# Kernel tuning notes

Hardware: AMD Instinct MI355X
Metric: run time of the kernel (lower is better)

Reference implementation:

```python
import jax, jax.numpy as jnp
import numpy as np
from jax import lax

DN = ('NCHW', 'OIHW', 'NCHW')

def conv2d(x, w, b=None, padding='SAME'):
    y = lax.conv_general_dilated(x, w, (1, 1), padding, dimension_numbers=DN)
    if b is not None:
        y = y + b[None, :, None, None]
    return y

def setup_inputs() -> dict:
    key = jax.random.key(0)
    ks = jax.random.split(key, 9)
    B, C, H, W = 8, 256, 64, 64
    s = lambda fan: 1.0 / np.sqrt(fan)
    return {
        'x': jax.random.normal(ks[0], (B, C, H, W), jnp.float32),
        'qkv_w': jax.random.normal(ks[1], (3 * C, C, 1, 1), jnp.float32) * s(C),
        'qkv_b': jnp.zeros((3 * C,), jnp.float32),
        'out_w': jax.random.normal(ks[2], (C, C, 1, 1), jnp.float32) * s(C),
        'out_b': jnp.zeros((C,), jnp.float32),
        'd1_w': jax.random.normal(ks[3], (8, 1, 3, 3), jnp.float32) * s(9),
        'd1_b': jnp.zeros((8,), jnp.float32),
        'd2_w': jax.random.normal(ks[4], (1, 8, 3, 3), jnp.float32) * s(72),
        'd2_b': jnp.zeros((1,), jnp.float32),
    }

def reference(x, qkv_w, qkv_b, out_w, out_b, d1_w, d1_b, d2_w, d2_b):
    B, C, H, W = x.shape
    N = H * W
    # gradient-energy (Laplacian) density proxy
    gray = x.mean(axis=1, keepdims=True)                      # [B,1,H,W]
    lap_k = jnp.array([[0., -1., 0.], [-1., 4., -1.], [0., -1., 0.]],
                      dtype=x.dtype).reshape(1, 1, 3, 3)
    lap = conv2d(gray, lap_k)                                 # [B,1,H,W]
    h = jax.nn.relu(conv2d(jnp.abs(lap), d1_w, d1_b))         # [B,8,H,W]
    density = jax.nn.sigmoid(conv2d(h, d2_w, d2_b))           # [B,1,H,W]
    # qkv via 1x1 conv == channel matmul
    qkv = jnp.einsum('oc,bchw->bohw', qkv_w[:, :, 0, 0], x) + qkv_b[None, :, None, None]
    q, k, v = jnp.split(qkv, 3, axis=1)                       # each [B,C,H,W]
    q = q.reshape(B, C, N).transpose(0, 2, 1)                 # [B,N,C]
    k = k.reshape(B, C, N)                                    # [B,C,N]
    v = v.reshape(B, C, N).transpose(0, 2, 1)                 # [B,N,C]
    attn = jnp.einsum('bnc,bcm->bnm', q, k) * (float(C) ** -0.5)  # [B,Nq,Nk]
    temperature = 1.0 + 2.0 * (1.0 - density.reshape(B, 1, N))    # per-key [B,1,Nk]
    attn = jax.nn.softmax(attn / temperature, axis=-1)
    out = jnp.einsum('bnm,bmc->bnc', attn, v)                 # [B,N,C]
    out = out.transpose(0, 2, 1).reshape(B, C, H, W)
    out = jnp.einsum('oc,bchw->bohw', out_w[:, :, 0, 0], out) + out_b[None, :, None, None]
    return out + x
```

## Files before the change

### kernel.cpp

```cpp
#include <hip/hip_runtime.h>
#include <hip/hip_bf16.h>

typedef __attribute__((ext_vector_type(8))) short s16x8;
typedef __attribute__((ext_vector_type(4))) float f32x4;
typedef __attribute__((ext_vector_type(4))) unsigned short us4;
typedef __attribute__((ext_vector_type(4))) unsigned int u32x4;

#define MFMA16(a,b,c) __builtin_amdgcn_mfma_f32_16x16x32_bf16((a),(b),(c),0,0,0)

__device__ __forceinline__ unsigned short f2b(float f){
  union{float f; unsigned u;} v; v.f = f;
  unsigned r = v.u + 0x7fffu + ((v.u>>16)&1u);
  return (unsigned short)(r>>16);
}

__device__ __forceinline__ void gl_lds16(const void* gp, void* lp){
  __builtin_amdgcn_global_load_lds((const __attribute__((address_space(1))) void*)gp,
                                   (__attribute__((address_space(3))) void*)lp, 16, 0, 0);
}

__device__ __forceinline__ void stage_64x256(void* lds, const unsigned short* g, int stride){
  const int t = threadIdx.x, wv = t>>6;
  #pragma unroll
  for (int i=0;i<8;++i){
    int ch = i*256 + t;
    int row = ch>>5, cc = ch&31, sc = cc ^ (row&7);
    gl_lds16((const char*)(g + (size_t)row*stride) + sc*16,
             (char*)lds + (((size_t)i*256 + wv*64)<<4));
  }
}
__device__ __forceinline__ void stage_256x64(void* lds, const unsigned short* g){
  const int t = threadIdx.x, wv = t>>6;
  #pragma unroll
  for (int i=0;i<8;++i){
    int ch = i*256 + t;
    int row = ch>>3, cc = ch&7, sc = cc ^ (row&7);
    gl_lds16((const char*)(g + (size_t)row*4096) + sc*16,
             (char*)lds + (((size_t)i*256 + wv*64)<<4));
  }
}

__global__ void k_cvt(const float* __restrict__ src, unsigned short* __restrict__ dst){
  int i = blockIdx.x*256 + threadIdx.x;
  f32x4 v = *(const f32x4*)(src + (size_t)i*4);
  us4 o;
  #pragma unroll
  for (int r=0;r<4;++r) o[r] = f2b(v[r]);
  *(us4*)(dst + (size_t)i*4) = o;
}

__global__ void k_gray(const float* __restrict__ xg, float* __restrict__ gray){
  int b = blockIdx.y, n = blockIdx.x*256 + threadIdx.x;
  const float* p = xg + (size_t)b*256*4096 + n;
  float s0=0,s1=0,s2=0,s3=0;
  for (int c=0;c<256;c+=4){
    s0 += p[(size_t)c*4096];
    s1 += p[(size_t)(c+1)*4096];
    s2 += p[(size_t)(c+2)*4096];
    s3 += p[(size_t)(c+3)*4096];
  }
  gray[b*4096+n] = (s0+s1+s2+s3)*(1.f/256.f);
}

__global__ void k_lapabs(const float* __restrict__ gray, float* __restrict__ labs){
  int b = blockIdx.y, n = blockIdx.x*256 + threadIdx.x;
  int hh = n>>6, ww = n&63;
  const float* g = gray + b*4096;
  float c = g[n];
  float up = hh>0  ? g[n-64] : 0.f;
  float dn = hh<63 ? g[n+64] : 0.f;
  float lf = ww>0  ? g[n-1]  : 0.f;
  float rt = ww<63 ? g[n+1]  : 0.f;
  labs[b*4096+n] = fabsf(4.f*c - up - dn - lf - rt);
}

__global__ void k_h8(const float* __restrict__ labs, const float* __restrict__ w1,
                     const float* __restrict__ b1, float* __restrict__ hbuf){
  int b = blockIdx.y, n = blockIdx.x*256 + threadIdx.x;
  int hh = n>>6, ww = n&63;
  const float* L = labs + b*4096;
  float tap[9];
  #pragma unroll
  for (int dy=-1;dy<=1;++dy)
    #pragma unroll
    for (int dx=-1;dx<=1;++dx){
      int y=hh+dy, x2=ww+dx;
      tap[(dy+1)*3+dx+1] = (y>=0&&y<64&&x2>=0&&x2<64)? L[y*64+x2] : 0.f;
    }
  #pragma unroll
  for (int j=0;j<8;++j){
    float a = b1[j];
    #pragma unroll
    for (int k=0;k<9;++k) a += w1[j*9+k]*tap[k];
    hbuf[((size_t)(b*8+j))*4096 + n] = fmaxf(a, 0.f);
  }
}

__global__ void k_scale(const float* __restrict__ hbuf, const float* __restrict__ w2,
                        const float* __restrict__ b2_, float* __restrict__ sc){
  int b = blockIdx.y, n = blockIdx.x*256 + threadIdx.x;
  int hh = n>>6, ww = n&63;
  float a = b2_[0];
  #pragma unroll
  for (int j=0;j<8;++j){
    const float* H = hbuf + ((size_t)(b*8+j))*4096;
    #pragma unroll
    for (int dy=-1;dy<=1;++dy)
      #pragma unroll
      for (int dx=-1;dx<=1;++dx){
        int y=hh+dy, x2=ww+dx;
        if (y>=0&&y<64&&x2>=0&&x2<64) a += w2[j*9+(dy+1)*3+(dx+1)]*H[y*64+x2];
      }
  }
  float sig = 1.f/(1.f+__expf(-a));
  sc[b*4096+n] = 0.0625f/(3.f - 2.f*sig);
}

__global__ void k_transpose(const float* __restrict__ xg, unsigned short* __restrict__ Xtg){
  __shared__ unsigned short T[64*68];
  const int nb = blockIdx.x, cb = blockIdx.y, b = blockIdx.z;
  const int n0 = nb*64, c0 = cb*64;
  const int t = threadIdx.x;
  #pragma unroll
  for (int i=0;i<4;++i){
    int idx = i*256 + t;
    int c = idx>>4, k4 = idx&15;
    f32x4 v = *(const f32x4*)(xg + ((size_t)(b*256 + c0 + c))*4096 + n0 + k4*4);
    us4 o;
    #pragma unroll
    for (int r=0;r<4;++r) o[r] = f2b(v[r]);
    *(us4*)&T[c*68 + k4*4] = o;
  }
  __syncthreads();
  #pragma unroll
  for (int i=0;i<2;++i){
    int idx = i*256 + t;
    int n = idx>>3, ck = idx&7;
    unsigned short vv[8];
    #pragma unroll
    for (int j=0;j<8;++j) vv[j] = T[(ck*8+j)*68 + n];
    *(u32x4*)(Xtg + ((size_t)(b*4096 + n0 + n))*256 + c0 + ck*8) = *(const u32x4*)vv;
  }
}

__global__ __launch_bounds__(256,2) void k_gemm_qkv(const unsigned short* __restrict__ Wg,
    const unsigned short* __restrict__ Xtg, const float* __restrict__ biasg,
    unsigned short* __restrict__ Qo, unsigned short* __restrict__ Ko, unsigned short* __restrict__ Vto){
  __shared__ unsigned short Wl[64*256], Xl[64*256];
  const int nt_ = blockIdx.x, at = blockIdx.y, b = blockIdx.z;
  const int a0 = at*64, n0 = nt_*64;
  stage_64x256(Wl, Wg + (size_t)a0*256, 256);
  stage_64x256(Xl, Xtg + ((size_t)(b*4096 + n0))*256, 256);
  __syncthreads();
  const int t = threadIdx.x, w = t>>6, lane = t&63, lam = lane&15, lg = lane>>4;
  f32x4 zz = {0.f,0.f,0.f,0.f};
  f32x4 acc[4] = {zz,zz,zz,zz};
  #pragma unroll
  for (int u=0;u<8;++u){
    int ar = 16*w + lam;
    s16x8 af = *(const s16x8*)((const char*)Wl + ar*512 + ((64*u+16*lg) ^ ((ar&7)<<4)));
    #pragma unroll
    for (int ct=0;ct<4;++ct){
      int br = 16*ct + lam;
      s16x8 bf = *(const s16x8*)((const char*)Xl + br*512 + ((64*u+16*lg) ^ ((br&7)<<4)));
      acc[ct] = MFMA16(af, bf, acc[ct]);
    }
  }
  const int ob = a0 + 16*w + 4*lg;
  f32x4 bias4 = *(const f32x4*)(biasg + ob);
  #pragma unroll
  for (int ct=0;ct<4;++ct){
    int n = n0 + 16*ct + lam;
    us4 ov;
    #pragma unroll
    for (int r=0;r<4;++r) ov[r] = f2b(acc[ct][r] + bias4[r]);
    if (a0 < 256){
      *(us4*)(Qo + ((size_t)(b*4096 + n))*256 + ob) = ov;
    } else if (a0 < 512){
      *(us4*)(Ko + ((size_t)(b*4096 + n))*256 + (ob-256)) = ov;
    } else {
      #pragma unroll
      for (int r=0;r<4;++r)
        Vto[((size_t)(b*256 + (ob-512+r)))*4096 + n] = ov[r];
    }
  }
}

__global__ __launch_bounds__(256,2) void k_attn(const unsigned short* __restrict__ Qg,
    const unsigned short* __restrict__ Kg, const unsigned short* __restrict__ Vtg,
    const float* __restrict__ Sg, unsigned short* __restrict__ AOt){
  __shared__ unsigned short Kl[64*256];
  __shared__ unsigned short Vl[256*64];
  __shared__ float sl[64];
  __shared__ __align__(16) char Pl[4][16*144];

  const int t = threadIdx.x, w = t>>6, lane = t&63, lam = lane&15, lg = lane>>4;
  const int b = blockIdx.x>>6, qt = blockIdx.x&63;
  const int qbase = qt*64 + w*16;

  s16x8 qf[8];
  {
    const unsigned short* qp = Qg + ((size_t)(b*4096 + qbase + lam))*256 + lg*8;
    #pragma unroll
    for (int u=0;u<8;++u) qf[u] = *(const s16x8*)(qp + 32*u);
  }
  f32x4 zz = {0.f,0.f,0.f,0.f};
  f32x4 oa[16];
  #pragma unroll
  for (int i=0;i<16;++i) oa[i] = zz;
  float m_run = -1.0e30f, l_run = 0.f;

  for (int kt=0; kt<64; ++kt){
    const int m0 = kt*64;
    if (kt) __syncthreads();
    stage_64x256(Kl, Kg + ((size_t)(b*4096 + m0))*256, 256);
    stage_256x64(Vl, Vtg + (size_t)b*256*4096 + m0);
    if (t < 64) sl[t] = Sg[(size_t)b*4096 + m0 + t];
    __syncthreads();

    f32x4 st[4] = {zz,zz,zz,zz};
    #pragma unroll
    for (int u=0;u<8;++u){
      #pragma unroll
      for (int mt=0;mt<4;++mt){
        int krow = 16*mt + lam;
        s16x8 kf = *(const s16x8*)((const char*)Kl + krow*512 + ((64*u + 16*lg) ^ ((krow&7)<<4)));
        st[mt] = MFMA16(kf, qf[u], st[mt]);
      }
    }
    float p[4][4]; float tmax = -1.0e30f;
    #pragma unroll
    for (int mt=0;mt<4;++mt){
      f32x4 s4 = *(const f32x4*)&sl[16*mt + 4*lg];
      #pragma unroll
      for (int r=0;r<4;++r){ p[mt][r] = st[mt][r]*s4[r]; tmax = fmaxf(tmax, p[mt][r]); }
    }
    tmax = fmaxf(tmax, __shfl_xor(tmax, 16));
    tmax = fmaxf(tmax, __shfl_xor(tmax, 32));
    float mnew = fmaxf(m_run, tmax);
    float fs = __expf(m_run - mnew);
    float rsum = 0.f;
    #pragma unroll
    for (int mt=0;mt<4;++mt){
      #pragma unroll
      for (int r=0;r<4;++r){ float e = __expf(p[mt][r]-mnew); p[mt][r]=e; rsum += e; }
    }
    rsum += __shfl_xor(rsum, 16);
    rsum += __shfl_xor(rsum, 32);
    l_run = l_run*fs + rsum; m_run = mnew;
    #pragma unroll
    for (int mt=0;mt<4;++mt){
      us4 pk;
      #pragma unroll
      for (int r=0;r<4;++r) pk[r] = f2b(p[mt][r]);
      *(us4*)(&Pl[w][0] + lam*144 + mt*32 + lg*8) = pk;
    }
    float fr[4];
    #pragma unroll
    for (int r=0;r<4;++r) fr[r] = __shfl(fs, 4*lg + r);
    #pragma unroll
    for (int i=0;i<16;++i){
      #pragma unroll
      for (int r=0;r<4;++r) oa[i][r] *= fr[r];
    }
    #pragma unroll
    for (int ks=0;ks<2;++ks){
      s16x8 pa = *(const s16x8*)(&Pl[w][0] + lam*144 + ks*64 + lg*16);
      #pragma unroll
      for (int ct=0;ct<16;++ct){
        int c = lam + 16*ct;
        s16x8 vf = *(const s16x8*)((const char*)Vl + c*128 + ((ks*64 + 16*lg) ^ ((c&7)<<4)));
        oa[ct] = MFMA16(pa, vf, oa[ct]);
      }
    }
  }
  float li = 1.f/l_run;
  float lr[4];
  #pragma unroll
  for (int r=0;r<4;++r) lr[r] = __shfl(li, 4*lg + r);
  #pragma unroll
  for (int ct=0;ct<16;++ct){
    #pragma unroll
    for (int r=0;r<4;++r){
      AOt[((size_t)(b*4096 + qbase + 4*lg + r))*256 + lam + 16*ct] = f2b(oa[ct][r]*lr[r]);
    }
  }
}

__global__ __launch_bounds__(256,2) void k_gemm_out(const unsigned short* __restrict__ Ag,
    const unsigned short* __restrict__ Bg, const float* __restrict__ biasg,
    const float* __restrict__ xg, float* __restrict__ outg){
  __shared__ unsigned short Al[64*256], Bl[64*256];
  const int at = blockIdx.x, bt = blockIdx.y, b = blockIdx.z;
  const int a0 = at*64, o0 = bt*64;
  stage_64x256(Al, Ag + ((size_t)(b*4096 + a0))*256, 256);
  stage_64x256(Bl, Bg + (size_t)o0*256, 256);
  __syncthreads();
  const int t = threadIdx.x, w = t>>6, lane = t&63, lam = lane&15, lg = lane>>4;
  f32x4 zz = {0.f,0.f,0.f,0.f};
  f32x4 acc[4] = {zz,zz,zz,zz};
  #pragma unroll
  for (int u=0;u<8;++u){
    int ar = 16*w + lam;
    s16x8 af = *(const s16x8*)((const char*)Al + ar*512 + ((64*u+16*lg) ^ ((ar&7)<<4)));
    #pragma unroll
    for (int ct=0;ct<4;++ct){
      int br = 16*ct + lam;
      s16x8 bf = *(const s16x8*)((const char*)Bl + br*512 + ((64*u+16*lg) ^ ((br&7)<<4)));
      acc[ct] = MFMA16(af, bf, acc[ct]);
    }
  }
  #pragma unroll
  for (int ct=0;ct<4;++ct){
    int o = o0 + 16*ct + lam;
    float ob_ = biasg[o];
    size_t base = ((size_t)(b*256 + o))*4096 + a0 + 16*w + 4*lg;
    f32x4 xv = *(const f32x4*)(xg + base);
    f32x4 ov;
    #pragma unroll
    for (int r=0;r<4;++r) ov[r] = acc[ct][r] + ob_ + xv[r];
    *(f32x4*)(outg + base) = ov;
  }
}

extern "C" void kernel_launch(void* const* d_in, const int* in_sizes, int n_in,
                              void* d_out, int out_size, void* d_ws, size_t ws_size,
                              hipStream_t stream){
  const float* x     = (const float*)d_in[0];
  const float* qkv_w = (const float*)d_in[1];
  const float* qkv_b = (const float*)d_in[2];
  const float* out_w = (const float*)d_in[3];
  const float* out_b = (const float*)d_in[4];
  const float* d1_w  = (const float*)d_in[5];
  const float* d1_b  = (const float*)d_in[6];
  const float* d2_w  = (const float*)d_in[7];
  const float* d2_b  = (const float*)d_in[8];
  float* out = (float*)d_out;

  char* p = (char*)d_ws;
  const size_t BIG = (size_t)8*4096*256*2;
  unsigned short* Xt = (unsigned short*)p; p += BIG;
  unsigned short* Q  = (unsigned short*)p; p += BIG;
  unsigned short* K  = (unsigned short*)p; p += BIG;
  unsigned short* Vt = (unsigned short*)p; p += BIG;
  unsigned short* Wq = (unsigned short*)p; p += (size_t)768*256*2;
  unsigned short* Wo = (unsigned short*)p; p += (size_t)256*256*2;
  float* gray = (float*)p; p += (size_t)8*4096*4;
  float* labs = (float*)p; p += (size_t)8*4096*4;
  float* hbuf = (float*)p; p += (size_t)8*8*4096*4;
  float* sc   = (float*)p; p += (size_t)8*4096*4;

  k_cvt      <<<dim3(192),    256, 0, stream>>>(qkv_w, Wq);
  k_cvt      <<<dim3(64),     256, 0, stream>>>(out_w, Wo);
  k_transpose<<<dim3(64,4,8), 256, 0, stream>>>(x, Xt);
  k_gray     <<<dim3(16,8),   256, 0, stream>>>(x, gray);
  k_lapabs   <<<dim3(16,8),   256, 0, stream>>>(gray, labs);
  k_h8       <<<dim3(16,8),   256, 0, stream>>>(labs, d1_w, d1_b, hbuf);
  k_scale    <<<dim3(16,8),   256, 0, stream>>>(hbuf, d2_w, d2_b, sc);
  k_gemm_qkv <<<dim3(64,12,8),256, 0, stream>>>(Wq, Xt, qkv_b, Q, K, Vt);
  k_attn     <<<dim3(512),    256, 0, stream>>>(Q, K, Vt, sc, Xt);
  k_gemm_out <<<dim3(64,4,8), 256, 0, stream>>>(Xt, Wo, out_b, x, out);
}
```

Baseline: 321.1 us.

## Split attention keys across two blocks with 32-row query tiles and merge partials

Each wave of the attention kernel now handles 32 query rows (two 16-row MFMA tiles) so every K/V fragment read from LDS feeds two MFMAs. The key range is split in half across paired blocks, which keeps the grid at 512 blocks. Each block writes partial normalized outputs plus running max and sum, and a new merge kernel combines them. The per-key scale is now read straight from global memory instead of LDS, and the P buffer uses an XOR swizzle. The costs are more registers per thread (two accumulator sets), an extra kernel launch, and extra global traffic for the partial outputs.

New measurement: 409.8 us. 27.6% more time.

```diff
diff --git a/kernel.cpp b/kernel.cpp
--- a/kernel.cpp
+++ b/kernel.cpp
@@ -8,6 +8,9 @@
 
 #define MFMA16(a,b,c) __builtin_amdgcn_mfma_f32_16x16x32_bf16((a),(b),(c),0,0,0)
 
+__device__ __forceinline__ float b2f(unsigned short u){
+  union{unsigned u; float f;} v; v.u = ((unsigned)u)<<16; return v.f;
+}
 __device__ __forceinline__ unsigned short f2b(float f){
   union{float f; unsigned u;} v; v.f = f;
   unsigned r = v.u + 0x7fffu + ((v.u>>16)&1u);
@@ -188,103 +191,197 @@
 
 __global__ __launch_bounds__(256,2) void k_attn(const unsigned short* __restrict__ Qg,
     const unsigned short* __restrict__ Kg, const unsigned short* __restrict__ Vtg,
-    const float* __restrict__ Sg, unsigned short* __restrict__ AOt){
+    const float* __restrict__ Sg, unsigned short* __restrict__ Opg, float* __restrict__ mlg){
   __shared__ unsigned short Kl[64*256];
   __shared__ unsigned short Vl[256*64];
-  __shared__ float sl[64];
-  __shared__ __align__(16) char Pl[4][16*144];
+  __shared__ __align__(16) unsigned short Pl[4][32*64];
 
   const int t = threadIdx.x, w = t>>6, lane = t&63, lam = lane&15, lg = lane>>4;
-  const int b = blockIdx.x>>6, qt = blockIdx.x&63;
-  const int qbase = qt*64 + w*16;
-
-  s16x8 qf[8];
+  const int bid = blockIdx.x;
+  const int b = bid>>6, qt = (bid>>1)&31, s = bid&1;
+  const int qbase = qt*128 + w*32;
+
+  s16x8 qf0[8], qf1[8];
   {
-    const unsigned short* qp = Qg + ((size_t)(b*4096 + qbase + lam))*256 + lg*8;
-    #pragma unroll
-    for (int u=0;u<8;++u) qf[u] = *(const s16x8*)(qp + 32*u);
+    const unsigned short* qp0 = Qg + ((size_t)(b*4096 + qbase + lam))*256 + lg*8;
+    const unsigned short* qp1 = qp0 + 16*256;
+    #pragma unroll
+    for (int u=0;u<8;++u){ qf0[u] = *(const s16x8*)(qp0 + 32*u); qf1[u] = *(const s16x8*)(qp1 + 32*u); }
   }
   f32x4 zz = {0.f,0.f,0.f,0.f};
-  f32x4 oa[16];
-  #pragma unroll
-  for (int i=0;i<16;++i) oa[i] = zz;
-  float m_run = -1.0e30f, l_run = 0.f;
-
-  for (int kt=0; kt<64; ++kt){
-    const int m0 = kt*64;
+  f32x4 oa0[16], oa1[16];
+  #pragma unroll
+  for (int i=0;i<16;++i){ oa0[i] = zz; oa1[i] = zz; }
+  float m_run0 = -1.0e30f, l_run0 = 0.f, m_run1 = -1.0e30f, l_run1 = 0.f;
+
+  for (int kt=0; kt<32; ++kt){
+    const int m0 = (s*32 + kt)*64;
     if (kt) __syncthreads();
     stage_64x256(Kl, Kg + ((size_t)(b*4096 + m0))*256, 256);
     stage_256x64(Vl, Vtg + (size_t)b*256*4096 + m0);
-    if (t < 64) sl[t] = Sg[(size_t)b*4096 + m0 + t];
     __syncthreads();
 
-    f32x4 st[4] = {zz,zz,zz,zz};
+    f32x4 st0[4] = {zz,zz,zz,zz}, st1[4] = {zz,zz,zz,zz};
     #pragma unroll
     for (int u=0;u<8;++u){
       #pragma unroll
       for (int mt=0;mt<4;++mt){
         int krow = 16*mt + lam;
         s16x8 kf = *(const s16x8*)((const char*)Kl + krow*512 + ((64*u + 16*lg) ^ ((krow&7)<<4)));
-        st[mt] = MFMA16(kf, qf[u], st[mt]);
-      }
-    }
-    float p[4][4]; float tmax = -1.0e30f;
-    #pragma unroll
-    for (int mt=0;mt<4;++mt){
-      f32x4 s4 = *(const f32x4*)&sl[16*mt + 4*lg];
-      #pragma unroll
-      for (int r=0;r<4;++r){ p[mt][r] = st[mt][r]*s4[r]; tmax = fmaxf(tmax, p[mt][r]); }
-    }
-    tmax = fmaxf(tmax, __shfl_xor(tmax, 16));
-    tmax = fmaxf(tmax, __shfl_xor(tmax, 32));
-    float mnew = fmaxf(m_run, tmax);
-    float fs = __expf(m_run - mnew);
-    float rsum = 0.f;
-    #pragma unroll
-    for (int mt=0;mt<4;++mt){
-      #pragma unroll
-      for (int r=0;r<4;++r){ float e = __expf(p[mt][r]-mnew); p[mt][r]=e; rsum += e; }
-    }
-    rsum += __shfl_xor(rsum, 16);
-    rsum += __shfl_xor(rsum, 32);
-    l_run = l_run*fs + rsum; m_run = mnew;
-    #pragma unroll
-    for (int mt=0;mt<4;++mt){
-      us4 pk;
-      #pragma unroll
-      for (int r=0;r<4;++r) pk[r] = f2b(p[mt][r]);
-      *(us4*)(&Pl[w][0] + lam*144 + mt*32 + lg*8) = pk;
-    }
-    float fr[4];
-    #pragma unroll
-    for (int r=0;r<4;++r) fr[r] = __shfl(fs, 4*lg + r);
-    #pragma unroll
-    for (int i=0;i<16;++i){
-      #pragma unroll
-      for (int r=0;r<4;++r) oa[i][r] *= fr[r];
+        st0[mt] = MFMA16(kf, qf0[u], st0[mt]);
+        st1[mt] = MFMA16(kf, qf1[u], st1[mt]);
+      }
+    }
+    {
+      float tmax = -1.0e30f;
+      #pragma unroll
+      for (int mt=0;mt<4;++mt){
+        f32x4 s4 = *(const f32x4*)(Sg + (size_t)b*4096 + m0 + 16*mt + 4*lg);
+        #pragma unroll
+        for (int r=0;r<4;++r){ st0[mt][r] *= s4[r]; tmax = fmaxf(tmax, st0[mt][r]); }
+      }
+      tmax = fmaxf(tmax, __shfl_xor(tmax,16));
+      tmax = fmaxf(tmax, __shfl_xor(tmax,32));
+      float mnew = fmaxf(m_run0, tmax);
+      float fs = __expf(m_run0 - mnew);
+      float rsum = 0.f;
+      #pragma unroll
+      for (int mt=0;mt<4;++mt){
+        #pragma unroll
+        for (int r=0;r<4;++r){ float e = __expf(st0[mt][r]-mnew); st0[mt][r]=e; rsum += e; }
+      }
+      rsum += __shfl_xor(rsum,16);
+      rsum += __shfl_xor(rsum,32);
+      l_run0 = l_run0*fs + rsum; m_run0 = mnew;
+      const int row = lam;
+      #pragma unroll
+      for (int mt=0;mt<4;++mt){
+        us4 pk;
+        #pragma unroll
+        for (int r=0;r<4;++r) pk[r] = f2b(st0[mt][r]);
+        *(us4*)((char*)&Pl[w][0] + row*128 + ((mt*32 + lg*8) ^ ((row&7)<<4))) = pk;
+      }
+      float fr[4];
+      #pragma unroll
+      for (int r=0;r<4;++r) fr[r] = __shfl(fs, 4*lg + r);
+      #pragma unroll
+      for (int i=0;i<16;++i){
+        #pragma unroll
+        for (int r=0;r<4;++r) oa0[i][r] *= fr[r];
+      }
+    }
+    {
+      float tmax = -1.0e30f;
+      #pragma unroll
+      for (int mt=0;mt<4;++mt){
+        f32x4 s4 = *(const f32x4*)(Sg + (size_t)b*4096 + m0 + 16*mt + 4*lg);
+        #pragma unroll
+        for (int r=0;r<4;++r){ st1[mt][r] *= s4[r]; tmax = fmaxf(tmax, st1[mt][r]); }
+      }
+      tmax = fmaxf(tmax, __shfl_xor(tmax,16));
+      tmax = fmaxf(tmax, __shfl_xor(tmax,32));
+      float mnew = fmaxf(m_run1, tmax);
+      float fs = __expf(m_run1 - mnew);
+      float rsum = 0.f;
+      #pragma unroll
+      for (int mt=0;mt<4;++mt){
+        #pragma unroll
+        for (int r=0;r<4;++r){ float e = __expf(st1[mt][r]-mnew); st1[mt][r]=e; rsum += e; }
+      }
+      rsum += __shfl_xor(rsum,16);
+      rsum += __shfl_xor(rsum,32);
+      l_run1 = l_run1*fs + rsum; m_run1 = mnew;
+      const int row = 16 + lam;
+      #pragma unroll
+      for (int mt=0;mt<4;++mt){
+        us4 pk;
+        #pragma unroll
+        for (int r=0;r<4;++r) pk[r] = f2b(st1[mt][r]);
+        *(us4*)((char*)&Pl[w][0] + row*128 + ((mt*32 + lg*8) ^ ((row&7)<<4))) = pk;
+      }
+      float fr[4];
+      #pragma unroll
+      for (int r=0;r<4;++r) fr[r] = __shfl(fs, 4*lg + r);
+      #pragma unroll
+      for (int i=0;i<16;++i){
+        #pragma unroll
+        for (int r=0;r<4;++r) oa1[i][r] *= fr[r];
+      }
     }
     #pragma unroll
     for (int ks=0;ks<2;++ks){
-      s16x8 pa = *(const s16x8*)(&Pl[w][0] + lam*144 + ks*64 + lg*16);
+      const int r0 = lam, r1 = 16 + lam;
+      s16x8 pa0 = *(const s16x8*)((const char*)&Pl[w][0] + r0*128 + ((ks*64 + lg*16) ^ ((r0&7)<<4)));
+      s16x8 pa1 = *(const s16x8*)((const char*)&Pl[w][0] + r1*128 + ((ks*64 + lg*16) ^ ((r1&7)<<4)));
       #pragma unroll
       for (int ct=0;ct<16;++ct){
         int c = lam + 16*ct;
         s16x8 vf = *(const s16x8*)((const char*)Vl + c*128 + ((ks*64 + 16*lg) ^ ((c&7)<<4)));
-        oa[ct] = MFMA16(pa, vf, oa[ct]);
-      }
-    }
-  }
-  float li = 1.f/l_run;
-  float lr[4];
-  #pragma unroll
-  for (int r=0;r<4;++r) lr[r] = __shfl(li, 4*lg + r);
-  #pragma unroll
-  for (int ct=0;ct<16;++ct){
-    #pragma unroll
-    for (int r=0;r<4;++r){
-      AOt[((size_t)(b*4096 + qbase + 4*lg + r))*256 + lam + 16*ct] = f2b(oa[ct][r]*lr[r]);
-    }
-  }
+        oa0[ct] = MFMA16(pa0, vf, oa0[ct]);
+        oa1[ct] = MFMA16(pa1, vf, oa1[ct]);
+      }
+    }
+  }
+  const size_t obase = ((size_t)(b*2 + s))*4096;
+  {
+    float li = 1.f/l_run0;
+    float lr[4];
+    #pragma unroll
+    for (int r=0;r<4;++r) lr[r] = __shfl(li, 4*lg + r);
+    #pragma unroll
+    for (int ct=0;ct<16;++ct){
+      #pragma unroll
+      for (int r=0;r<4;++r)
+        Opg[(obase + qbase + 4*lg + r)*256 + lam + 16*ct] = f2b(oa0[ct][r]*lr[r]);
+    }
+    if (lane < 16){
+      mlg[(obase + qbase + lam)*2]     = m_run0;
+      mlg[(obase + qbase + lam)*2 + 1] = l_run0;
+    }
+  }
+  {
+    float li = 1.f/l_run1;
+    float lr[4];
+    #pragma unroll
+    for (int r=0;r<4;++r) lr[r] = __shfl(li, 4*lg + r);
+    #pragma unroll
+    for (int ct=0;ct<16;++ct){
+      #pragma unroll
+      for (int r=0;r<4;++r)
+        Opg[(obase + qbase + 16 + 4*lg + r)*256 + lam + 16*ct] = f2b(oa1[ct][r]*lr[r]);
+    }
+    if (lane < 16){
+      mlg[(obase + qbase + 16 + lam)*2]     = m_run1;
+      mlg[(obase + qbase + 16 + lam)*2 + 1] = l_run1;
+    }
+  }
+}
+
+__global__ void k_merge(const unsigned short* __restrict__ Opg, const float* __restrict__ mlg,
+                        unsigned short* __restrict__ AOt){
+  int rr = blockIdx.x*8 + (threadIdx.x>>5);
+  int b = rr>>12, n = rr&4095;
+  int c0 = (threadIdx.x&31)*8;
+  size_t base0 = ((size_t)(b*2+0))*4096 + n;
+  size_t base1 = ((size_t)(b*2+1))*4096 + n;
+  float m0 = mlg[base0*2], l0 = mlg[base0*2+1];
+  float m1 = mlg[base1*2], l1 = mlg[base1*2+1];
+  float M = fmaxf(m0,m1);
+  float w0 = __expf(m0-M)*l0, w1 = __expf(m1-M)*l1;
+  float inv = 1.f/(w0+w1);
+  w0 *= inv; w1 *= inv;
+  u32x4 a = *(const u32x4*)(Opg + base0*256 + c0);
+  u32x4 c = *(const u32x4*)(Opg + base1*256 + c0);
+  u32x4 o;
+  #pragma unroll
+  for (int k=0;k<4;++k){
+    float alo = b2f((unsigned short)(a[k]&0xffffu)), ahi = b2f((unsigned short)(a[k]>>16));
+    float clo = b2f((unsigned short)(c[k]&0xffffu)), chi = b2f((unsigned short)(c[k]>>16));
+    unsigned lo = f2b(w0*alo + w1*clo);
+    unsigned hi = f2b(w0*ahi + w1*chi);
+    o[k] = lo | (hi<<16);
+  }
+  *(u32x4*)(AOt + ((size_t)(b*4096+n))*256 + c0) = o;
 }
 
 __global__ __launch_bounds__(256,2) void k_gemm_out(const unsigned short* __restrict__ Ag,
@@ -349,6 +446,8 @@
   float* labs = (float*)p; p += (size_t)8*4096*4;
   float* hbuf = (float*)p; p += (size_t)8*8*4096*4;
   float* sc   = (float*)p; p += (size_t)8*4096*4;
+  unsigned short* Op = (unsigned short*)p; p += (size_t)8*2*4096*256*2;
+  float* ml = (float*)p; p += (size_t)8*2*4096*2*4;
 
   k_cvt      <<<dim3(192),    256, 0, stream>>>(qkv_w, Wq);
   k_cvt      <<<dim3(64),     256, 0, stream>>>(out_w, Wo);
@@ -358,6 +457,7 @@
   k_h8       <<<dim3(16,8),   256, 0, stream>>>(labs, d1_w, d1_b, hbuf);
   k_scale    <<<dim3(16,8),   256, 0, stream>>>(hbuf, d2_w, d2_b, sc);
   k_gemm_qkv <<<dim3(64,12,8),256, 0, stream>>>(Wq, Xt, qkv_b, Q, K, Vt);
-  k_attn     <<<dim3(512),    256, 0, stream>>>(Q, K, Vt, sc, Xt);
+  k_attn     <<<dim3(512),    256, 0, stream>>>(Q, K, Vt, sc, Op, ml);
+  k_merge    <<<dim3(4096),   256, 0, stream>>>(Op, ml, Xt);
   k_gemm_out <<<dim3(64,4,8), 256, 0, stream>>>(Xt, Wo, out_b, x, out);
 }
```

## Double-buffer K/V tiles in attention with 512-thread blocks and swizzled P

Applied to the files above, without the earlier changes.

The attention kernel now uses 8 waves per block covering 128 queries and splits K/V staging across 512 threads. K/V tiles are double-buffered in LDS so the next tile's global-to-LDS load overlaps the current tile's MFMA work, leaving one barrier per iteration. The per-key scale is read directly from global memory instead of LDS, the P buffer uses an XOR swizzle instead of padding, and the MFMA sections are wrapped in s_setprio. LDS use grows to about 132KB per block and the grid halves to 256 blocks, which may cut occupancy to one block per CU.

Measured after the change: 325.8 us. Within noise of the previous version (+1.5%).

```diff
diff --git a/kernel.cpp b/kernel.cpp
--- a/kernel.cpp
+++ b/kernel.cpp
@@ -8,6 +8,9 @@
 
 #define MFMA16(a,b,c) __builtin_amdgcn_mfma_f32_16x16x32_bf16((a),(b),(c),0,0,0)
 
+__device__ __forceinline__ float b2f(unsigned short u){
+  union{unsigned u; float f;} v; v.u = ((unsigned)u)<<16; return v.f;
+}
 __device__ __forceinline__ unsigned short f2b(float f){
   union{float f; unsigned u;} v; v.f = f;
   unsigned r = v.u + 0x7fffu + ((v.u>>16)&1u);
@@ -29,14 +32,24 @@
              (char*)lds + (((size_t)i*256 + wv*64)<<4));
   }
 }
-__device__ __forceinline__ void stage_256x64(void* lds, const unsigned short* g){
+__device__ __forceinline__ void stage_K512(void* lds, const unsigned short* g){
   const int t = threadIdx.x, wv = t>>6;
   #pragma unroll
-  for (int i=0;i<8;++i){
-    int ch = i*256 + t;
+  for (int i=0;i<4;++i){
+    int ch = i*512 + t;
+    int row = ch>>5, cc = ch&31, sc = cc ^ (row&7);
+    gl_lds16((const char*)g + (size_t)row*512 + sc*16,
+             (char*)lds + (((size_t)i*512 + wv*64)<<4));
+  }
+}
+__device__ __forceinline__ void stage_V512(void* lds, const unsigned short* g){
+  const int t = threadIdx.x, wv = t>>6;
+  #pragma unroll
+  for (int i=0;i<4;++i){
+    int ch = i*512 + t;
     int row = ch>>3, cc = ch&7, sc = cc ^ (row&7);
     gl_lds16((const char*)(g + (size_t)row*4096) + sc*16,
-             (char*)lds + (((size_t)i*256 + wv*64)<<4));
+             (char*)lds + (((size_t)i*512 + wv*64)<<4));
   }
 }
 
@@ -186,17 +199,17 @@
   }
 }
 
-__global__ __launch_bounds__(256,2) void k_attn(const unsigned short* __restrict__ Qg,
+__global__ __launch_bounds__(512,2) void k_attn(const unsigned short* __restrict__ Qg,
     const unsigned short* __restrict__ Kg, const unsigned short* __restrict__ Vtg,
     const float* __restrict__ Sg, unsigned short* __restrict__ AOt){
-  __shared__ unsigned short Kl[64*256];
-  __shared__ unsigned short Vl[256*64];
-  __shared__ float sl[64];
-  __shared__ __align__(16) char Pl[4][16*144];
+  __shared__ unsigned short Kl[2][64*256];
+  __shared__ unsigned short Vl[2][256*64];
+  __shared__ __align__(16) unsigned short Pl[8][16*64];
 
   const int t = threadIdx.x, w = t>>6, lane = t&63, lam = lane&15, lg = lane>>4;
-  const int b = blockIdx.x>>6, qt = blockIdx.x&63;
-  const int qbase = qt*64 + w*16;
+  const int bid = blockIdx.x;
+  const int b = bid&7, qt = bid>>3;
+  const int qbase = qt*128 + w*16;
 
   s16x8 qf[8];
   {
@@ -210,50 +223,64 @@
   for (int i=0;i<16;++i) oa[i] = zz;
   float m_run = -1.0e30f, l_run = 0.f;
 
+  const unsigned short* Kb = Kg + (size_t)b*4096*256;
+  const unsigned short* Vb = Vtg + (size_t)b*256*4096;
+
+  stage_K512(&Kl[0][0], Kb);
+  stage_V512(&Vl[0][0], Vb);
+  __syncthreads();
+
+  int cur = 0;
   for (int kt=0; kt<64; ++kt){
     const int m0 = kt*64;
-    if (kt) __syncthreads();
-    stage_64x256(Kl, Kg + ((size_t)(b*4096 + m0))*256, 256);
-    stage_256x64(Vl, Vtg + (size_t)b*256*4096 + m0);
-    if (t < 64) sl[t] = Sg[(size_t)b*4096 + m0 + t];
-    __syncthreads();
+    if (kt < 63){
+      stage_K512(&Kl[cur^1][0], Kb + (size_t)(m0+64)*256);
+      stage_V512(&Vl[cur^1][0], Vb + (m0+64));
+    }
+    f32x4 s4[4];
+    #pragma unroll
+    for (int mt=0;mt<4;++mt) s4[mt] = *(const f32x4*)(Sg + (size_t)b*4096 + m0 + 16*mt + 4*lg);
 
     f32x4 st[4] = {zz,zz,zz,zz};
+    const char* Kc = (const char*)&Kl[cur][0];
+    __builtin_amdgcn_s_setprio(1);
     #pragma unroll
     for (int u=0;u<8;++u){
       #pragma unroll
       for (int mt=0;mt<4;++mt){
         int krow = 16*mt + lam;
-        s16x8 kf = *(const s16x8*)((const char*)Kl + krow*512 + ((64*u + 16*lg) ^ ((krow&7)<<4)));
+        s16x8 kf = *(const s16x8*)(Kc + krow*512 + ((64*u + 16*lg) ^ ((krow&7)<<4)));
         st[mt] = MFMA16(kf, qf[u], st[mt]);
       }
     }
-    float p[4][4]; float tmax = -1.0e30f;
+    __builtin_amdgcn_s_setprio(0);
+
+    float tmax = -1.0e30f;
     #pragma unroll
     for (int mt=0;mt<4;++mt){
-      f32x4 s4 = *(const f32x4*)&sl[16*mt + 4*lg];
-      #pragma unroll
-      for (int r=0;r<4;++r){ p[mt][r] = st[mt][r]*s4[r]; tmax = fmaxf(tmax, p[mt][r]); }
-    }
-    tmax = fmaxf(tmax, __shfl_xor(tmax, 16));
-    tmax = fmaxf(tmax, __shfl_xor(tmax, 32));
+      #pragma unroll
+      for (int r=0;r<4;++r){ st[mt][r] *= s4[mt][r]; tmax = fmaxf(tmax, st[mt][r]); }
+    }
+    tmax = fmaxf(tmax, __shfl_xor(tmax,16));
+    tmax = fmaxf(tmax, __shfl_xor(tmax,32));
     float mnew = fmaxf(m_run, tmax);
     float fs = __expf(m_run - mnew);
     float rsum = 0.f;
     #pragma unroll
     for (int mt=0;mt<4;++mt){
       #pragma unroll
-      for (int r=0;r<4;++r){ float e = __expf(p[mt][r]-mnew); p[mt][r]=e; rsum += e; }
-    }
-    rsum += __shfl_xor(rsum, 16);
-    rsum += __shfl_xor(rsum, 32);
+      for (int r=0;r<4;++r){ float e = __expf(st[mt][r]-mnew); st[mt][r]=e; rsum += e; }
+    }
+    rsum += __shfl_xor(rsum,16);
+    rsum += __shfl_xor(rsum,32);
     l_run = l_run*fs + rsum; m_run = mnew;
+
     #pragma unroll
     for (int mt=0;mt<4;++mt){
       us4 pk;
       #pragma unroll
-      for (int r=0;r<4;++r) pk[r] = f2b(p[mt][r]);
-      *(us4*)(&Pl[w][0] + lam*144 + mt*32 + lg*8) = pk;
+      for (int r=0;r<4;++r) pk[r] = f2b(st[mt][r]);
+      *(us4*)((char*)&Pl[w][0] + lam*128 + ((mt*32 + lg*8) ^ ((lam&7)<<4))) = pk;
     }
     float fr[4];
     #pragma unroll
@@ -263,16 +290,22 @@
       #pragma unroll
       for (int r=0;r<4;++r) oa[i][r] *= fr[r];
     }
+    const char* Vc = (const char*)&Vl[cur][0];
+    __builtin_amdgcn_s_setprio(1);
     #pragma unroll
     for (int ks=0;ks<2;++ks){
-      s16x8 pa = *(const s16x8*)(&Pl[w][0] + lam*144 + ks*64 + lg*16);
+      s16x8 pa = *(const s16x8*)((const char*)&Pl[w][0] + lam*128 + ((ks*64 + lg*16) ^ ((lam&7)<<4)));
       #pragma unroll
       for (int ct=0;ct<16;++ct){
         int c = lam + 16*ct;
-        s16x8 vf = *(const s16x8*)((const char*)Vl + c*128 + ((ks*64 + 16*lg) ^ ((c&7)<<4)));
+        s16x8 vf = *(const s16x8*)(Vc + c*128 + ((ks*64 + 16*lg) ^ ((c&7)<<4)));
         oa[ct] = MFMA16(pa, vf, oa[ct]);
       }
     }
+    __builtin_amdgcn_s_setprio(0);
+
+    __syncthreads();
+    cur ^= 1;
   }
   float li = 1.f/l_run;
   float lr[4];
@@ -358,6 +391,6 @@
   k_h8       <<<dim3(16,8),   256, 0, stream>>>(labs, d1_w, d1_b, hbuf);
   k_scale    <<<dim3(16,8),   256, 0, stream>>>(hbuf, d2_w, d2_b, sc);
   k_gemm_qkv <<<dim3(64,12,8),256, 0, stream>>>(Wq, Xt, qkv_b, Q, K, Vt);
-  k_attn     <<<dim3(512),    256, 0, stream>>>(Q, K, Vt, sc, Xt);
+  k_attn     <<<dim3(256),    512, 0, stream>>>(Q, K, Vt, sc, Xt);
   k_gemm_out <<<dim3(64,4,8), 256, 0, stream>>>(Xt, Wo, out_b, x, out);
 }
```
